# Kernel tuning notes

Hardware: AMD Instinct MI355X
Metric: run time of the kernel (lower is better)

The kernel has to match this reference:

```python
import jax, jax.numpy as jnp
import numpy as np

PC_LO = jnp.array([-50.0, -50.0, -5.0], jnp.float32)
PC_HI = jnp.array([50.0, 50.0, 3.0], jnp.float32)
IMG_H, IMG_W = 256, 704
G, P, L = 1, 8, 4
C_FEAT = 132  # 128 feat + 3 pos_3d + 1 uncertainty
ALPHA, EPS = 0.1, 1e-6


def conv2d(x, w, b, pad):
    y = jax.lax.conv_general_dilated(x, w, (1, 1), [(pad, pad), (pad, pad)],
                                     dimension_numbers=('NCHW', 'OIHW', 'NCHW'))
    return y + b[None, :, None, None]


def inorm(x, eps=1e-5):
    m = x.mean(axis=(2, 3), keepdims=True)
    v = ((x - m) ** 2).mean(axis=(2, 3), keepdims=True)
    return (x - m) * jax.lax.rsqrt(v + eps)


def bilinear_sample(feat, gx, gy):
    # feat [C,H,W]; gx,gy [Q] in [-1,1]; align_corners=False, zero padding
    C, H, W = feat.shape
    x = (gx + 1.0) * 0.5 * W - 0.5
    y = (gy + 1.0) * 0.5 * H - 0.5
    x0 = jnp.floor(x)
    y0 = jnp.floor(y)
    wx1 = x - x0
    wy1 = y - y0

    def tap(xi, yi, wgt):
        ok = (xi >= 0) & (xi < W) & (yi >= 0) & (yi < H)
        xi_c = jnp.clip(xi, 0, W - 1).astype(jnp.int32)
        yi_c = jnp.clip(yi, 0, H - 1).astype(jnp.int32)
        return feat[:, yi_c, xi_c] * (wgt * ok)[None, :]

    return (tap(x0, y0, (1 - wx1) * (1 - wy1)) + tap(x0 + 1, y0, wx1 * (1 - wy1))
            + tap(x0, y0 + 1, (1 - wx1) * wy1) + tap(x0 + 1, y0 + 1, wx1 * wy1))


def reference(bev_query, bev_pos, lidar2img, feat0, feat1, feat2, feat3,
              in_w, in_b, off_w, off_b, sw_w, sw_b,
              mid_w1, mid_b1, mid_w2, mid_b2, mid_w3, mid_b3, out_w, out_b):
    b, _, h, w = bev_query.shape
    hw = h * w
    scale = 1.0
    # in_conv + InstanceNorm
    q = bev_query + conv2d(bev_query, in_w, in_b, 2)
    q = inorm(q)
    # sampling offsets: b (g p 3) h w -> b (h w) g p 3
    off = jax.nn.sigmoid(conv2d(q, off_w, off_b, 0))
    off = off.reshape(b, G, P, 3, h, w).transpose(0, 4, 5, 1, 2, 3).reshape(b, hw, G, P, 3)
    rng = 0.25 * scale + EPS
    off = jnp.concatenate([off[..., :2] * rng * 2 - rng,
                           off[..., 2:3] * (4.0 + EPS) * 2 - (4.0 + EPS)], axis=-1)
    # reference points: normalized bev_pos -> metric + offsets
    ref = bev_pos.reshape(b, hw, 1, 1, 3) * (PC_HI - PC_LO) + PC_LO
    ref = ref + off  # [b, hw, g, p, 3]
    # scale weights: b (g p l) h w -> b (h w) g 1 p l, softmax over l
    sw = conv2d(q, sw_w, sw_b, 0).reshape(b, G, P, L, h, w)
    sw = sw.transpose(0, 4, 5, 1, 2, 3).reshape(b, hw, G, P, L)[:, :, :, None]
    sw = jax.nn.softmax(sw, axis=-1)
    # sampling_4d: project 3D points to each camera
    pts = jnp.concatenate([ref, jnp.ones(ref.shape[:-1] + (1,), ref.dtype)], axis=-1)
    cam = jnp.einsum('bnij,bqgpj->bnqgpi', lidar2img, pts)  # [b,n,hw,g,p,4]
    z = cam[..., 2]
    valid = z > 1e-5
    xy = cam[..., :2] / jnp.maximum(z, 1e-5)[..., None]
    gx = jnp.where(valid, xy[..., 0] / IMG_W * 2 - 1, -2.0)
    gy = jnp.where(valid, xy[..., 1] / IMG_H * 2 - 1, -2.0)
    n = lidar2img.shape[1]
    Q = hw * G * P
    gxf = gx.reshape(b * n, Q)
    gyf = gy.reshape(b * n, Q)
    sampled = jnp.zeros((b, n, hw, G, P, C_FEAT), ref.dtype)
    for l, feat in enumerate((feat0, feat1, feat2, feat3)):
        ff = feat.reshape(b * n, C_FEAT, feat.shape[3], feat.shape[4])
        s = jax.vmap(bilinear_sample)(ff, gxf, gyf)  # [bn, C, Q]
        s = s.reshape(b, n, C_FEAT, hw, G, P).transpose(0, 1, 3, 4, 5, 2)
        wl = sw[:, :, :, 0, :, l]  # [b, hw, g, p]
        sampled = sampled + s * wl[:, None, :, :, :, None]
    sampled = sampled.sum(axis=1)  # sum over cameras -> [b, hw, g, p, C_FEAT]
    # split: 128 features, 3 pos_3d, 1 uncertainty
    feats128 = sampled[..., :128]
    pos3d = sampled[..., 128:131]
    dist = jnp.linalg.norm(ref - pos3d, axis=-1)
    wgt = jnp.exp(-ALPHA * dist ** 2)[..., None]
    weighted = feats128 * wgt

    def fold(x):  # b (h w) g p c -> b p (g c) h w -> sum over p
        return x.reshape(b, h, w, G * P, 128).sum(axis=3).transpose(0, 3, 1, 2)

    sf = jnp.concatenate([fold(feats128), fold(weighted)], axis=1)  # [b,256,h,w]
    m = jax.nn.gelu(conv2d(sf, mid_w1, mid_b1, 1), approximate=False)
    m = jax.nn.gelu(conv2d(m, mid_w2, mid_b2, 0), approximate=False)
    q = q + conv2d(m, mid_w3, mid_b3, 1)
    q = inorm(q)
    q = q + conv2d(q, out_w, out_b, 2)
    q = inorm(q)
    return q


def setup_inputs():
    key = jax.random.key(0)
    ks = jax.random.split(key, 32)
    f32 = jnp.float32
    d = {}
    d['bev_query'] = jax.random.normal(ks[0], (1, 128, 100, 100), f32)
    d['bev_pos'] = jax.random.uniform(ks[1], (1, 100, 100, 3), f32)
    d['lidar2img'] = jax.random.normal(ks[2], (1, 6, 4, 4), f32)
    lvl_shapes = [(32, 88), (16, 44), (8, 22), (4, 11)]
    for i, (hh, ww) in enumerate(lvl_shapes):
        d['feat%d' % i] = jax.random.normal(ks[3 + i], (1, 6, C_FEAT, hh, ww), f32)

    def W(k, shape):
        return jax.random.normal(k, shape, f32) * 0.05

    d['in_w'] = W(ks[10], (128, 128, 5, 5)); d['in_b'] = W(ks[11], (128,))
    d['off_w'] = W(ks[12], (G * P * 3, 128, 1, 1))
    d['off_b'] = jax.random.uniform(ks[13], (G * P * 3,), f32, -2.0, 2.0)
    d['sw_w'] = W(ks[14], (G * P * L, 128, 1, 1)); d['sw_b'] = W(ks[15], (G * P * L,))
    d['mid_w1'] = W(ks[16], (512, 256, 3, 3)); d['mid_b1'] = W(ks[17], (512,))
    d['mid_w2'] = W(ks[18], (512, 512, 1, 1)); d['mid_b2'] = W(ks[19], (512,))
    d['mid_w3'] = W(ks[20], (128, 512, 3, 3)); d['mid_b3'] = W(ks[21], (128,))
    d['out_w'] = W(ks[22], (128, 128, 5, 5)); d['out_b'] = W(ks[23], (128,))
    return d
```

## Files before the change

kernel.cpp:

```cpp
#include <hip/hip_runtime.h>
#include <cstddef>


#define HW   10000
#define WID  100

typedef __attribute__((ext_vector_type(8))) __bf16 bf16x8;
typedef __attribute__((ext_vector_type(4))) float f32x4;
typedef __attribute__((ext_vector_type(4))) unsigned int uint4v;

#define AS1 __attribute__((address_space(1)))
#define AS3 __attribute__((address_space(3)))

__device__ __forceinline__ float gelu_exact(float x) {
    return 0.5f * x * (1.0f + erff(x * 0.7071067811865475f));
}
__device__ __forceinline__ unsigned short f2bf(float v) {
    unsigned int b = __float_as_uint(v);
    return (unsigned short)((b + 0x7FFFu + ((b >> 16) & 1u)) >> 16);
}
__device__ __forceinline__ float bf2f(short s) {
    return __uint_as_float(((unsigned int)(unsigned short)s) << 16);
}
__device__ __forceinline__ bf16x8 load_frag(const short* p) {
    return __builtin_bit_cast(bf16x8, *(const uint4v*)p);
}

template<int CIN, int KS, int COUT, int EPI, bool ACT, int OPAD, int OPW, int KSPLIT>
__global__ __launch_bounds__(256)
void mfma_conv(const short* __restrict__ wpk, const short* __restrict__ xcl,
               const float* __restrict__ bias,
               float* __restrict__ outcm, short* __restrict__ outcl)
{
    constexpr int PW = 100 + 2 * (KS / 2);
    constexpr int CHUNK = (KS + KSPLIT - 1) / KSPLIT;
    constexpr int CINB = CIN / 32;
    __shared__ short As[8192];
    __shared__ short Bs[8192];

    const int t    = threadIdx.x;
    const int lane = t & 63;
    const int wv   = t >> 6;
    const int wr = wv >> 1;
    const int wc = wv & 1;
    const int lq = lane >> 4;
    const int ln = lane & 15;

    const int oc0 = blockIdx.x * 128;
    const int y0  = blockIdx.y * 4;
    const int zb  = blockIdx.z;
    const int bx  = (KSPLIT > 1) ? (zb & 3) : zb;
    const int ks  = (KSPLIT > 1) ? (zb >> 2) : 0;
    const int x0  = bx * 32;
    const int ky_lo = ks * CHUNK;
    const int ky_hi = (ky_lo + CHUNK < KS) ? ky_lo + CHUNK : KS;

    const int srow  = t >> 2;
    const int sslot = (t & 3) * 8;

    const int nsteps = (ky_hi - ky_lo) * KS * CINB;

    f32x4 acc[4][4];
#pragma unroll
    for (int mt = 0; mt < 4; ++mt)
#pragma unroll
        for (int nt = 0; nt < 4; ++nt)
#pragma unroll
            for (int r = 0; r < 4; ++r) acc[mt][nt][r] = 0.f;

    auto stage = [&](int b, int s) {
        const int ky  = ky_lo + s / (KS * CINB);
        const int rem = s % (KS * CINB);
        const int kx  = rem / CINB;
        const int ic0 = (rem % CINB) * 32;
        const short* wsl = wpk + (size_t)((ky * KS + kx) * COUT + oc0) * CIN + ic0 + sslot;
        const short* xsl = xcl + (size_t)(ky * PW + kx) * CIN + ic0 + sslot;
#pragma unroll
        for (int i = 0; i < 2; ++i) {
            const int row = i * 64 + srow;
            const short* ga = wsl + (size_t)row * CIN;
            __builtin_amdgcn_global_load_lds(
                (const AS1 unsigned int*)ga,
                (AS3 unsigned int*)((AS3 char*)As + b * 8192 + i * 4096 + wv * 1024),
                16, 0, 0);
        }
#pragma unroll
        for (int i = 0; i < 2; ++i) {
            const int np = i * 64 + srow;
            const short* gb = xsl + (size_t)((y0 + (np >> 5)) * PW + x0 + (np & 31)) * CIN;
            __builtin_amdgcn_global_load_lds(
                (const AS1 unsigned int*)gb,
                (AS3 unsigned int*)((AS3 char*)Bs + b * 8192 + i * 4096 + wv * 1024),
                16, 0, 0);
        }
    };

    stage(0, 0);
    __syncthreads();

    int cur = 0;
    for (int s = 0; s < nsteps; ++s) {
        if (s + 1 < nsteps) stage(cur ^ 1, s + 1);

        const short* ab = As + cur * 4096;
        const short* bb = Bs + cur * 4096;
        bf16x8 a[4], b[4];
#pragma unroll
        for (int mt = 0; mt < 4; ++mt)
            a[mt] = load_frag(ab + (wr * 64 + mt * 16 + ln) * 32 + lq * 8);
#pragma unroll
        for (int nt = 0; nt < 4; ++nt)
            b[nt] = load_frag(bb + (wc * 64 + nt * 16 + ln) * 32 + lq * 8);
#pragma unroll
        for (int mt = 0; mt < 4; ++mt)
#pragma unroll
            for (int nt = 0; nt < 4; ++nt)
                acc[mt][nt] = __builtin_amdgcn_mfma_f32_16x16x32_bf16(
                    a[mt], b[nt], acc[mt][nt], 0, 0, 0);

        __syncthreads();
        cur ^= 1;
    }

#pragma unroll
    for (int mt = 0; mt < 4; ++mt) {
        const int ocr = oc0 + wr * 64 + mt * 16 + lq * 4;
        float bb[4];
        if (EPI == 1) {
            const float4 bv = *(const float4*)(bias + ocr);
            bb[0] = bv.x; bb[1] = bv.y; bb[2] = bv.z; bb[3] = bv.w;
        }
#pragma unroll
        for (int nt = 0; nt < 4; ++nt) {
            const int nl = wc * 64 + nt * 16 + ln;
            const int x = x0 + (nl & 31);
            const int y = y0 + (nl >> 5);
            if (x >= 100) continue;
            if (EPI == 1) {
                float v[4];
#pragma unroll
                for (int r = 0; r < 4; ++r) {
                    float tv = acc[mt][nt][r] + bb[r];
                    if (ACT) tv = gelu_exact(tv);
                    v[r] = tv;
                }
                ushort4 pk;
                pk.x = f2bf(v[0]); pk.y = f2bf(v[1]); pk.z = f2bf(v[2]); pk.w = f2bf(v[3]);
                *(ushort4*)(outcl + ((size_t)(y + OPAD) * OPW + (x + OPAD)) * COUT + ocr) = pk;
            } else {
                const int pix = y * WID + x;
#pragma unroll
                for (int r = 0; r < 4; ++r)
                    outcm[((size_t)ks * COUT + ocr + r) * HW + pix] = acc[mt][nt][r];
            }
        }
    }
}

template<int NS>
__global__ __launch_bounds__(256)
void red_norm_k(const float* __restrict__ bias, const float* __restrict__ res,
                const float* __restrict__ slab, float* __restrict__ outp)
{
    const int c = blockIdx.x, tid = threadIdx.x;
    const size_t base = (size_t)c * HW;
    const float bc = bias[c];
    float v[40];
    float s1 = 0.f, s2 = 0.f;
#pragma unroll
    for (int k = 0; k < 40; ++k) {
        const int i = tid + k * 256;
        float x = 0.f;
        if (i < HW) {
            x = bc + res[base + i];
#pragma unroll
            for (int z = 0; z < NS; ++z) x += slab[(size_t)z * 1280000 + base + i];
            s1 += x; s2 += x * x;
        }
        v[k] = x;
    }
    __shared__ float r1[256], r2[256];
    r1[tid] = s1; r2[tid] = s2; __syncthreads();
    for (int o = 128; o > 0; o >>= 1) {
        if (tid < o) { r1[tid] += r1[tid + o]; r2[tid] += r2[tid + o]; }
        __syncthreads();
    }
    const float mean = r1[0] * 1e-4f;
    const float var  = fmaxf(r2[0] * 1e-4f - mean * mean, 0.f);
    const float rstd = rsqrtf(var + 1e-5f);
#pragma unroll
    for (int k = 0; k < 40; ++k) {
        const int i = tid + k * 256;
        if (i < HW) outp[base + i] = (v[k] - mean) * rstd;
    }
}

__global__ void pad_cat_x(const float* __restrict__ in, short* __restrict__ out)
{
    const int total = 10816 * 384;
    for (int i = blockIdx.x * blockDim.x + threadIdx.x; i < total; i += gridDim.x * blockDim.x) {
        const int c = i % 384;
        const int p = i / 384;
        const int x = p % 104 - 2;
        const int y = p / 104 - 2;
        const int sc = c & 127;
        float v = 0.f;
        if (x >= 0 && x < 100 && y >= 0 && y < 100) v = in[(size_t)sc * HW + y * WID + x];
        const unsigned short hi = f2bf(v);
        short o;
        if (c >= 128 && c < 256) o = (short)f2bf(v - bf2f((short)hi));
        else                     o = (short)hi;
        out[i] = o;
    }
}

__global__ void pack_w1_cat(const float* __restrict__ w, short* __restrict__ out)
{
    const int total = 25 * 128 * 384;
    for (int i = blockIdx.x * blockDim.x + threadIdx.x; i < total; i += gridDim.x * blockDim.x) {
        const int c = i % 384;
        int t = i / 384;
        const int oc = t % 128;
        const int s = t / 128;
        const int ky = s / 5, kx = s % 5;
        const int sc = c & 127;
        const float v = w[(((size_t)oc * 128 + sc) * 5 + ky) * 5 + kx];
        const unsigned short hi = f2bf(v);
        out[i] = (c < 256) ? (short)hi : (short)f2bf(v - bf2f((short)hi));
    }
}

template<int C, int PAD>
__global__ void pad_cl_cast(const float* __restrict__ in, short* __restrict__ out)
{
    constexpr int PW = 100 + 2 * PAD;
    const int total = PW * PW * C;
    for (int i = blockIdx.x * blockDim.x + threadIdx.x; i < total; i += gridDim.x * blockDim.x) {
        const int c = i % C;
        const int p = i / C;
        const int x = p % PW - PAD;
        const int y = p / PW - PAD;
        float v = 0.f;
        if (x >= 0 && x < 100 && y >= 0 && y < 100) v = in[(size_t)c * HW + y * WID + x];
        out[i] = (short)f2bf(v);
    }
}

__global__ void pack_all_bf16(const float* __restrict__ w1, const float* __restrict__ w2,
                              const float* __restrict__ w3, const float* __restrict__ w4,
                              short* __restrict__ out)
{
    const int E0 = 1179648, E1 = E0 + 262144, E2 = E1 + 589824, E3 = E2 + 409600;
    for (int i = blockIdx.x * blockDim.x + threadIdx.x; i < E3; i += gridDim.x * blockDim.x) {
        const float* w; int OC, CI, KS, j;
        if (i < E0)      { w = w1; OC = 512; CI = 256; KS = 3; j = i; }
        else if (i < E1) { w = w2; OC = 512; CI = 512; KS = 1; j = i - E0; }
        else if (i < E2) { w = w3; OC = 128; CI = 512; KS = 3; j = i - E1; }
        else             { w = w4; OC = 128; CI = 128; KS = 5; j = i - E2; }
        const int ic = j % CI;
        int t = j / CI;
        const int oc = t % OC;
        const int s = t / OC;
        const int ky = s / KS, kx = s % KS;
        out[i] = (short)f2bf(w[(((size_t)oc * CI + ic) * KS + ky) * KS + kx]);
    }
}

__global__ void transpose_all(const float* __restrict__ f0, const float* __restrict__ f1,
                              const float* __restrict__ f2, const float* __restrict__ f3,
                              short* __restrict__ out)
{
    const int O1 = 2230272, O2 = O1 + 557568, O3 = O2 + 139392, O4 = O3 + 34848;
    for (int i = blockIdx.x * blockDim.x + threadIdx.x; i < O4; i += gridDim.x * blockDim.x) {
        const float* f; int Hl, Wl, j;
        if (i < O1)      { f = f0; Hl = 32; Wl = 88; j = i; }
        else if (i < O2) { f = f1; Hl = 16; Wl = 44; j = i - O1; }
        else if (i < O3) { f = f2; Hl = 8;  Wl = 22; j = i - O2; }
        else             { f = f3; Hl = 4;  Wl = 11; j = i - O3; }
        const int c = j % 132;
        int t = j / 132;
        const int x = t % Wl; t /= Wl;
        const int y = t % Hl; t /= Hl;
        const int n = t;
        out[i] = (short)f2bf(f[(((size_t)n * 132 + c) * Hl + y) * Wl + x]);
    }
}

__global__ __launch_bounds__(64)
void offsw_proj(const float* __restrict__ qn, const float* __restrict__ bev_pos,
                const float* __restrict__ off_w, const float* __restrict__ off_b,
                const float* __restrict__ sw_w, const float* __restrict__ sw_b,
                const float* __restrict__ l2i,
                float* __restrict__ refp, float* __restrict__ swts,
                float2* __restrict__ recs, int* __restrict__ recn, int* __restrict__ cnts)
{
    const int pix = blockIdx.x;
    const int tid = threadIdx.x;
    __shared__ float qv[128];
    __shared__ float swraw[32];
    __shared__ float rp[24];
    qv[tid]      = qn[(size_t)tid * HW + pix];
    qv[tid + 64] = qn[(size_t)(tid + 64) * HW + pix];
    __syncthreads();

    if (tid < 24) {
        float acc = off_b[tid];
        for (int c = 0; c < 128; ++c) acc = fmaf(qv[c], off_w[tid * 128 + c], acc);
        const float s = 1.0f / (1.0f + expf(-acc));
        const int coord = tid % 3;
        const float rng = (coord < 2) ? 0.250001f : 4.000001f;
        const float v = s * rng * 2.0f - rng;
        const float lo[3]   = {-50.f, -50.f, -5.f};
        const float span[3] = {100.f, 100.f, 8.f};
        const float rv = bev_pos[pix * 3 + coord] * span[coord] + lo[coord] + v;
        refp[pix * 24 + tid] = rv;
        rp[tid] = rv;
    } else if (tid >= 32) {
        const int j = tid - 32;
        float acc = sw_b[j];
        for (int c = 0; c < 128; ++c) acc = fmaf(qv[c], sw_w[j * 128 + c], acc);
        swraw[j] = acc;
    }
    __syncthreads();
    if (tid < 8) {
        float m = -1e30f;
#pragma unroll
        for (int l = 0; l < 4; ++l) m = fmaxf(m, swraw[tid * 4 + l]);
        float e[4], sum = 0.f;
#pragma unroll
        for (int l = 0; l < 4; ++l) { e[l] = expf(swraw[tid * 4 + l] - m); sum += e[l]; }
        const float inv = 1.0f / sum;
#pragma unroll
        for (int l = 0; l < 4; ++l) swts[pix * 32 + tid * 4 + l] = e[l] * inv;
    }

    bool keep = false;
    float gx = -2.f, gy = -2.f;
    int p = 0, n = 0;
    if (tid < 48) {
        p = tid / 6;
        n = tid - p * 6;
        const float X = rp[p * 3 + 0], Y = rp[p * 3 + 1], Z = rp[p * 3 + 2];
        const float* m = l2i + n * 16;
        const float cx = m[0] * X + m[1] * Y + m[2]  * Z + m[3];
        const float cy = m[4] * X + m[5] * Y + m[6]  * Z + m[7];
        const float cz = m[8] * X + m[9] * Y + m[10] * Z + m[11];
        const bool valid = cz > 1e-5f;
        const float zz = fmaxf(cz, 1e-5f);
        gx = valid ? (cx / zz) * (2.0f / 704.0f) - 1.0f : -2.0f;
        gy = valid ? (cy / zz) * (2.0f / 256.0f) - 1.0f : -2.0f;
        keep = (gx > -1.092f) && (gx < 1.092f) && (gy > -1.26f) && (gy < 1.26f);
    }
    const unsigned long long bm = __ballot(keep);
    if (keep) {
        const unsigned long long gmask = 0x3Full << (p * 6);
        const int slot = __popcll(bm & ((1ull << tid) - 1ull) & gmask);
        recs[(size_t)pix * 48 + p * 6 + slot] = make_float2(gx, gy);
        recn[(size_t)pix * 48 + p * 6 + slot] = n;
    }
    if (tid < 48 && (tid % 6) == 0) {
        const unsigned long long gmask = 0x3Full << (p * 6);
        cnts[pix * 8 + p] = __popcll(bm & gmask);
    }
}

__global__ __launch_bounds__(64)
void sample_k4(const float* __restrict__ refp, const float* __restrict__ swts,
               const float2* __restrict__ recs, const int* __restrict__ recn,
               const int* __restrict__ cnts,
               const short* __restrict__ fb0,
               short* __restrict__ sfo)
{
    const int pix = blockIdx.x;
    const int tid = threadIdx.x;
    const int c0  = tid * 2;
    __shared__ float rp[24], sw[32], tail[32];
    __shared__ float2 rec[48];
    __shared__ int rn[48];
    __shared__ int cnt[8];
    __shared__ int4   toff[192];
    __shared__ float4 twt[192];
    if (tid < 24) rp[tid] = refp[pix * 24 + tid];
    if (tid < 32) sw[tid] = swts[pix * 32 + tid];
    if (tid < 48) { rec[tid] = recs[(size_t)pix * 48 + tid]; rn[tid] = recn[(size_t)pix * 48 + tid]; }
    if (tid < 8)  cnt[tid] = cnts[pix * 8 + tid];
    __syncthreads();

    const int HL[4] = {32, 16, 8, 4};
    const int WL[4] = {88, 44, 22, 11};
    const int LB[4] = {0, 2230272, 2787840, 2927232};

    for (int e = tid; e < 192; e += 64) {
        const int p  = e / 24;
        const int rl = e - p * 24;
        const int r  = rl >> 2;
        const int l  = rl & 3;
        int4 off = make_int4(0, 0, 0, 0);
        float4 wt = make_float4(0.f, 0.f, 0.f, 0.f);
        if (r < cnt[p]) {
            const float gx = rec[p * 6 + r].x;
            const float gy = rec[p * 6 + r].y;
            const int   n  = rn[p * 6 + r];
            const float wl = sw[p * 4 + l];
            const int Hl = HL[l], Wl = WL[l];
            const float fx = (gx + 1.0f) * 0.5f * (float)Wl - 0.5f;
            const float fy = (gy + 1.0f) * 0.5f * (float)Hl - 0.5f;
            if (fx >= -1.0f && fx < (float)Wl && fy >= -1.0f && fy < (float)Hl) {
                const float x0f = floorf(fx), y0f = floorf(fy);
                const int x0 = (int)x0f, y0 = (int)y0f;
                const int x1 = x0 + 1, y1 = y0 + 1;
                const float wx1 = fx - x0f, wy1 = fy - y0f;
                const float wx0 = 1.0f - wx1, wy0 = 1.0f - wy1;
                const bool okx0 = (x0 >= 0), okx1 = (x1 < Wl);
                const bool oky0 = (y0 >= 0), oky1 = (y1 < Hl);
                const int xc0 = okx0 ? x0 : 0, xc1 = okx1 ? x1 : Wl - 1;
                const int yc0 = oky0 ? y0 : 0, yc1 = oky1 ? y1 : Hl - 1;
                const int base = LB[l] + n * Hl * Wl * 132;
                off.x = base + (yc0 * Wl + xc0) * 132;
                off.y = base + (yc0 * Wl + xc1) * 132;
                off.z = base + (yc1 * Wl + xc0) * 132;
                off.w = base + (yc1 * Wl + xc1) * 132;
                wt.x = (okx0 && oky0) ? wx0 * wy0 * wl : 0.f;
                wt.y = (okx1 && oky0) ? wx1 * wy0 * wl : 0.f;
                wt.z = (okx0 && oky1) ? wx0 * wy1 * wl : 0.f;
                wt.w = (okx1 && oky1) ? wx1 * wy1 * wl : 0.f;
            }
        }
        toff[e] = off;
        twt[e]  = wt;
    }
    __syncthreads();

#define LOADB(L, W, P, R)                                                        \
    do {                                                                         \
        const int eb_ = (P) * 24 + (R) * 4;                                      \
        _Pragma("unroll")                                                        \
        for (int l = 0; l < 4; ++l) {                                            \
            const int4 offv_ = toff[eb_ + l];                                    \
            W[l] = twt[eb_ + l];                                                 \
            const int ox_ = __builtin_amdgcn_readfirstlane(offv_.x);             \
            const int oy_ = __builtin_amdgcn_readfirstlane(offv_.y);             \
            const int oz_ = __builtin_amdgcn_readfirstlane(offv_.z);             \
            const int ow_ = __builtin_amdgcn_readfirstlane(offv_.w);             \
            L[l * 4 + 0] = *(const unsigned int*)(fb0 + ox_ + c0);               \
            L[l * 4 + 1] = *(const unsigned int*)(fb0 + oy_ + c0);               \
            L[l * 4 + 2] = *(const unsigned int*)(fb0 + oz_ + c0);               \
            L[l * 4 + 3] = *(const unsigned int*)(fb0 + ow_ + c0);               \
        }                                                                        \
    } while (0)

#define FMAB(L, W)                                                               \
    do {                                                                         \
        _Pragma("unroll")                                                        \
        for (int l = 0; l < 4; ++l) {                                            \
            a0.x = fmaf(__uint_as_float(L[l * 4 + 0] << 16),          W[l].x, a0.x); \
            a0.y = fmaf(__uint_as_float(L[l * 4 + 0] & 0xFFFF0000u),  W[l].x, a0.y); \
            a1.x = fmaf(__uint_as_float(L[l * 4 + 1] << 16),          W[l].y, a1.x); \
            a1.y = fmaf(__uint_as_float(L[l * 4 + 1] & 0xFFFF0000u),  W[l].y, a1.y); \
            a2.x = fmaf(__uint_as_float(L[l * 4 + 2] << 16),          W[l].z, a2.x); \
            a2.y = fmaf(__uint_as_float(L[l * 4 + 2] & 0xFFFF0000u),  W[l].z, a2.y); \
            a3.x = fmaf(__uint_as_float(L[l * 4 + 3] << 16),          W[l].w, a3.x); \
            a3.y = fmaf(__uint_as_float(L[l * 4 + 3] & 0xFFFF0000u),  W[l].w, a3.y); \
        }                                                                        \
    } while (0)

    float2 acc[8];
#pragma unroll
    for (int p = 0; p < 8; ++p) {
        float2 a0 = {0.f, 0.f}, a1 = {0.f, 0.f}, a2 = {0.f, 0.f}, a3 = {0.f, 0.f};
        const int c = cnt[p];
        unsigned int LA[16]; float4 WA[4];
        if (c > 0) LOADB(LA, WA, p, 0);
        int r = 0;
        while (r < c) {
            unsigned int LB2[16]; float4 WB[4];
            if (r + 1 < c) LOADB(LB2, WB, p, r + 1);
            FMAB(LA, WA);
            ++r;
            if (r >= c) break;
            if (r + 1 < c) LOADB(LA, WA, p, r + 1);
            FMAB(LB2, WB);
            ++r;
        }
        acc[p].x = (a0.x + a1.x) + (a2.x + a3.x);
        acc[p].y = (a0.y + a1.y) + (a2.y + a3.y);
    }
#undef LOADB
#undef FMAB

    {
        const int p   = tid >> 3;
        const int sub = tid & 7;
        const int c   = cnt[p];
        const int nslots = c * 16;
        float t0 = 0.f, t1 = 0.f, t2 = 0.f;
        for (int s = sub; s < nslots; s += 8) {
            const int e  = p * 24 + (s >> 2);
            const int tp = s & 3;
            const int4   offv = toff[e];
            const float4 wtv  = twt[e];
            const int   off = (tp == 0) ? offv.x : (tp == 1) ? offv.y : (tp == 2) ? offv.z : offv.w;
            const float w   = (tp == 0) ? wtv.x  : (tp == 1) ? wtv.y  : (tp == 2) ? wtv.z  : wtv.w;
            const uint2 u = *(const uint2*)(fb0 + off + 128);
            t0 = fmaf(__uint_as_float(u.x << 16),         w, t0);
            t1 = fmaf(__uint_as_float(u.x & 0xFFFF0000u), w, t1);
            t2 = fmaf(__uint_as_float(u.y << 16),         w, t2);
        }
#pragma unroll
        for (int o = 4; o > 0; o >>= 1) {
            t0 += __shfl_down(t0, o, 8);
            t1 += __shfl_down(t1, o, 8);
            t2 += __shfl_down(t2, o, 8);
        }
        if (sub == 0) {
            tail[p * 4 + 0] = t0;
            tail[p * 4 + 1] = t1;
            tail[p * 4 + 2] = t2;
        }
    }
    __syncthreads();

    float2 sf1 = {0.f, 0.f}, sf2 = {0.f, 0.f};
#pragma unroll
    for (int p = 0; p < 8; ++p) {
        const float dx = rp[p * 3]     - tail[p * 4 + 0];
        const float dy = rp[p * 3 + 1] - tail[p * 4 + 1];
        const float dz = rp[p * 3 + 2] - tail[p * 4 + 2];
        const float wgt = expf(-0.1f * (dx * dx + dy * dy + dz * dz));
        sf1.x += acc[p].x;  sf1.y += acc[p].y;
        sf2.x += acc[p].x * wgt;  sf2.y += acc[p].y * wgt;
    }
    const int y = pix / WID, x = pix % WID;
    const size_t po = ((size_t)(y + 1) * 102 + (x + 1)) * 256;
    ushort2 p1; p1.x = f2bf(sf1.x); p1.y = f2bf(sf1.y);
    ushort2 p2; p2.x = f2bf(sf2.x); p2.y = f2bf(sf2.y);
    *(ushort2*)(sfo + po + c0)       = p1;
    *(ushort2*)(sfo + po + 128 + c0) = p2;
}


extern "C" void kernel_launch(void* const* d_in, const int* in_sizes, int n_in,
                              void* d_out, int out_size, void* d_ws, size_t ws_size,
                              hipStream_t stream)
{
    const float* bev_query = (const float*)d_in[0];
    const float* bev_pos   = (const float*)d_in[1];
    const float* l2i       = (const float*)d_in[2];
    const float* feat0     = (const float*)d_in[3];
    const float* feat1     = (const float*)d_in[4];
    const float* feat2     = (const float*)d_in[5];
    const float* feat3     = (const float*)d_in[6];
    const float* in_w      = (const float*)d_in[7];
    const float* in_b      = (const float*)d_in[8];
    const float* off_w     = (const float*)d_in[9];
    const float* off_b     = (const float*)d_in[10];
    const float* sw_w      = (const float*)d_in[11];
    const float* sw_b      = (const float*)d_in[12];
    const float* mid_w1    = (const float*)d_in[13];
    const float* mid_b1    = (const float*)d_in[14];
    const float* mid_w2    = (const float*)d_in[15];
    const float* mid_b2    = (const float*)d_in[16];
    const float* mid_w3    = (const float*)d_in[17];
    const float* mid_b3    = (const float*)d_in[18];
    const float* out_w     = (const float*)d_in[19];
    const float* out_b     = (const float*)d_in[20];
    float* out = (float*)d_out;

    float* ws    = (float*)d_ws;
    float* qn    = ws;
    float* refp  = qn + 1280000;
    float* swts  = refp + 240000;
    float* E     = swts + 320000;
    float* F     = E + 6400000;
    float* H     = F + 1800000;
    short* wp_all= (short*)(H + 2700000);

    float*  slab  = E;
    short*  fT0   = (short*)E;
    float2* recs  = (float2*)(E + 1600000);
    int*    recn  = (int*)(E + 2560000);
    int*    cnts  = (int*)(E + 3040000);
    short*  m1_cl = (short*)E;
    short*  xcat  = (short*)F;
    short*  wcat  = (short*)(F + 2100000);
    short*  sf_cl = (short*)F;
    short*  q2pad = (short*)F;
    short*  m2_cl = (short*)H;
    short*  wp_m1 = wp_all;
    short*  wp_m2 = wp_m1 + 1179648;
    short*  wp_m3 = wp_m2 + 262144;
    short*  wp_out= wp_m3 + 589824;

    const dim3 blk(256);

    hipLaunchKernelGGL(pack_w1_cat, dim3(1200), blk, 0, stream, in_w, wcat);
    hipLaunchKernelGGL(pack_all_bf16, dim3(9536), blk, 0, stream,
                       mid_w1, mid_w2, mid_w3, out_w, wp_all);

    hipLaunchKernelGGL(pad_cat_x, dim3(4056), blk, 0, stream, bev_query, xcat);
    hipLaunchKernelGGL((mfma_conv<384, 5, 128, 2, false, 0, 0, 5>), dim3(1, 25, 20), blk, 0, stream,
                       wcat, xcat, in_b, slab, nullptr);
    hipLaunchKernelGGL(red_norm_k<5>, dim3(128), blk, 0, stream, in_b, bev_query, slab, qn);

    hipLaunchKernelGGL(offsw_proj, dim3(HW), dim3(64), 0, stream,
                       qn, bev_pos, off_w, off_b, sw_w, sw_b, l2i,
                       refp, swts, recs, recn, cnts);

    hipLaunchKernelGGL(transpose_all, dim3(11571), blk, 0, stream,
                       feat0, feat1, feat2, feat3, fT0);

    hipMemsetAsync(sf_cl, 0, (size_t)2663424 * 2, stream);
    hipLaunchKernelGGL(sample_k4, dim3(HW), dim3(64), 0, stream,
                       refp, swts, recs, recn, cnts, fT0, sf_cl);

    hipLaunchKernelGGL((mfma_conv<256, 3, 512, 1, true, 0, 100, 1>), dim3(4, 25, 4), blk, 0, stream,
                       wp_m1, sf_cl, mid_b1, nullptr, m1_cl);
    hipMemsetAsync(m2_cl, 0, (size_t)5326848 * 2, stream);
    hipLaunchKernelGGL((mfma_conv<512, 1, 512, 1, true, 1, 102, 1>), dim3(4, 25, 4), blk, 0, stream,
                       wp_m2, m1_cl, mid_b2, nullptr, m2_cl);
    hipLaunchKernelGGL((mfma_conv<512, 3, 128, 2, false, 0, 0, 3>), dim3(1, 25, 12), blk, 0, stream,
                       wp_m3, m2_cl, mid_b3, slab, nullptr);
    hipLaunchKernelGGL(red_norm_k<3>, dim3(128), blk, 0, stream, mid_b3, qn, slab, qn);
    hipLaunchKernelGGL((pad_cl_cast<128, 2>), dim3(5411), blk, 0, stream, qn, q2pad);
    hipLaunchKernelGGL((mfma_conv<128, 5, 128, 2, false, 0, 0, 5>), dim3(1, 25, 20), blk, 0, stream,
                       wp_out, q2pad, out_b, slab, nullptr);
    hipLaunchKernelGGL(red_norm_k<5>, dim3(128), blk, 0, stream, out_b, qn, slab, out);
}
```

Before: 528.0 us.

## Halve conv pixel tile to two rows and interleave sampling of two points

The MFMA conv template gains an NT parameter. All five conv launches now use a 2-row pixel tile (64 pixels) instead of 4 rows, which doubles the grid, halves accumulator registers and B-tile LDS, and should raise occupancy on a 256-CU part. In exchange, weight tiles are reloaded twice as often per output. Separately, the sampling kernel processes two sampling points per loop iteration with interleaved loads and FMAs for more memory-level parallelism. It also reads weights from LDS at FMA time instead of holding them in registers.

```diff
diff --git a/kernel.cpp b/kernel.cpp
--- a/kernel.cpp
+++ b/kernel.cpp
@@ -26,7 +26,7 @@
     return __builtin_bit_cast(bf16x8, *(const uint4v*)p);
 }
 
-template<int CIN, int KS, int COUT, int EPI, bool ACT, int OPAD, int OPW, int KSPLIT>
+template<int CIN, int KS, int COUT, int EPI, bool ACT, int OPAD, int OPW, int KSPLIT, int NT>
 __global__ __launch_bounds__(256)
 void mfma_conv(const short* __restrict__ wpk, const short* __restrict__ xcl,
                const float* __restrict__ bias,
@@ -35,8 +35,9 @@
     constexpr int PW = 100 + 2 * (KS / 2);
     constexpr int CHUNK = (KS + KSPLIT - 1) / KSPLIT;
     constexpr int CINB = CIN / 32;
+    constexpr int BBUF = NT * 2048;
     __shared__ short As[8192];
-    __shared__ short Bs[8192];
+    __shared__ short Bs[NT * 2048];
 
     const int t    = threadIdx.x;
     const int lane = t & 63;
@@ -47,7 +48,7 @@
     const int ln = lane & 15;
 
     const int oc0 = blockIdx.x * 128;
-    const int y0  = blockIdx.y * 4;
+    const int y0  = blockIdx.y * NT;
     const int zb  = blockIdx.z;
     const int bx  = (KSPLIT > 1) ? (zb & 3) : zb;
     const int ks  = (KSPLIT > 1) ? (zb >> 2) : 0;
@@ -60,11 +61,11 @@
 
     const int nsteps = (ky_hi - ky_lo) * KS * CINB;
 
-    f32x4 acc[4][4];
+    f32x4 acc[4][NT];
 #pragma unroll
     for (int mt = 0; mt < 4; ++mt)
 #pragma unroll
-        for (int nt = 0; nt < 4; ++nt)
+        for (int nt = 0; nt < NT; ++nt)
 #pragma unroll
             for (int r = 0; r < 4; ++r) acc[mt][nt][r] = 0.f;
 
@@ -85,12 +86,12 @@
                 16, 0, 0);
         }
 #pragma unroll
-        for (int i = 0; i < 2; ++i) {
+        for (int i = 0; i < NT / 2; ++i) {
             const int np = i * 64 + srow;
             const short* gb = xsl + (size_t)((y0 + (np >> 5)) * PW + x0 + (np & 31)) * CIN;
             __builtin_amdgcn_global_load_lds(
                 (const AS1 unsigned int*)gb,
-                (AS3 unsigned int*)((AS3 char*)Bs + b * 8192 + i * 4096 + wv * 1024),
+                (AS3 unsigned int*)((AS3 char*)Bs + b * BBUF + i * 4096 + wv * 1024),
                 16, 0, 0);
         }
     };
@@ -103,18 +104,18 @@
         if (s + 1 < nsteps) stage(cur ^ 1, s + 1);
 
         const short* ab = As + cur * 4096;
-        const short* bb = Bs + cur * 4096;
-        bf16x8 a[4], b[4];
+        const short* bb = Bs + cur * (NT * 1024);
+        bf16x8 a[4], b[NT];
 #pragma unroll
         for (int mt = 0; mt < 4; ++mt)
             a[mt] = load_frag(ab + (wr * 64 + mt * 16 + ln) * 32 + lq * 8);
 #pragma unroll
-        for (int nt = 0; nt < 4; ++nt)
-            b[nt] = load_frag(bb + (wc * 64 + nt * 16 + ln) * 32 + lq * 8);
+        for (int nt = 0; nt < NT; ++nt)
+            b[nt] = load_frag(bb + (wc * (NT * 16) + nt * 16 + ln) * 32 + lq * 8);
 #pragma unroll
         for (int mt = 0; mt < 4; ++mt)
 #pragma unroll
-            for (int nt = 0; nt < 4; ++nt)
+            for (int nt = 0; nt < NT; ++nt)
                 acc[mt][nt] = __builtin_amdgcn_mfma_f32_16x16x32_bf16(
                     a[mt], b[nt], acc[mt][nt], 0, 0, 0);
 
@@ -131,8 +132,8 @@
             bb[0] = bv.x; bb[1] = bv.y; bb[2] = bv.z; bb[3] = bv.w;
         }
 #pragma unroll
-        for (int nt = 0; nt < 4; ++nt) {
-            const int nl = wc * 64 + nt * 16 + ln;
+        for (int nt = 0; nt < NT; ++nt) {
+            const int nl = wc * (NT * 16) + nt * 16 + ln;
             const int x = x0 + (nl & 31);
             const int y = y0 + (nl >> 5);
             if (x >= 100) continue;
@@ -431,13 +432,12 @@
     }
     __syncthreads();
 
-#define LOADB(L, W, P, R)                                                        \
+#define LOADD(L, P, R)                                                           \
     do {                                                                         \
         const int eb_ = (P) * 24 + (R) * 4;                                      \
         _Pragma("unroll")                                                        \
         for (int l = 0; l < 4; ++l) {                                            \
             const int4 offv_ = toff[eb_ + l];                                    \
-            W[l] = twt[eb_ + l];                                                 \
             const int ox_ = __builtin_amdgcn_readfirstlane(offv_.x);             \
             const int oy_ = __builtin_amdgcn_readfirstlane(offv_.y);             \
             const int oz_ = __builtin_amdgcn_readfirstlane(offv_.z);             \
@@ -449,44 +449,51 @@
         }                                                                        \
     } while (0)
 
-#define FMAB(L, W)                                                               \
+#define FMAW(A0, A1, A2, A3, L, P, R)                                            \
     do {                                                                         \
+        const int eb_ = (P) * 24 + (R) * 4;                                      \
         _Pragma("unroll")                                                        \
         for (int l = 0; l < 4; ++l) {                                            \
-            a0.x = fmaf(__uint_as_float(L[l * 4 + 0] << 16),          W[l].x, a0.x); \
-            a0.y = fmaf(__uint_as_float(L[l * 4 + 0] & 0xFFFF0000u),  W[l].x, a0.y); \
-            a1.x = fmaf(__uint_as_float(L[l * 4 + 1] << 16),          W[l].y, a1.x); \
-            a1.y = fmaf(__uint_as_float(L[l * 4 + 1] & 0xFFFF0000u),  W[l].y, a1.y); \
-            a2.x = fmaf(__uint_as_float(L[l * 4 + 2] << 16),          W[l].z, a2.x); \
-            a2.y = fmaf(__uint_as_float(L[l * 4 + 2] & 0xFFFF0000u),  W[l].z, a2.y); \
-            a3.x = fmaf(__uint_as_float(L[l * 4 + 3] << 16),          W[l].w, a3.x); \
-            a3.y = fmaf(__uint_as_float(L[l * 4 + 3] & 0xFFFF0000u),  W[l].w, a3.y); \
+            const float4 w_ = twt[eb_ + l];                                      \
+            A0.x = fmaf(__uint_as_float(L[l * 4 + 0] << 16),          w_.x, A0.x); \
+            A0.y = fmaf(__uint_as_float(L[l * 4 + 0] & 0xFFFF0000u),  w_.x, A0.y); \
+            A1.x = fmaf(__uint_as_float(L[l * 4 + 1] << 16),          w_.y, A1.x); \
+            A1.y = fmaf(__uint_as_float(L[l * 4 + 1] & 0xFFFF0000u),  w_.y, A1.y); \
+            A2.x = fmaf(__uint_as_float(L[l * 4 + 2] << 16),          w_.z, A2.x); \
+            A2.y = fmaf(__uint_as_float(L[l * 4 + 2] & 0xFFFF0000u),  w_.z, A2.y); \
+            A3.x = fmaf(__uint_as_float(L[l * 4 + 3] << 16),          w_.w, A3.x); \
+            A3.y = fmaf(__uint_as_float(L[l * 4 + 3] & 0xFFFF0000u),  w_.w, A3.y); \
         }                                                                        \
     } while (0)
 
     float2 acc[8];
 #pragma unroll
-    for (int p = 0; p < 8; ++p) {
-        float2 a0 = {0.f, 0.f}, a1 = {0.f, 0.f}, a2 = {0.f, 0.f}, a3 = {0.f, 0.f};
-        const int c = cnt[p];
-        unsigned int LA[16]; float4 WA[4];
-        if (c > 0) LOADB(LA, WA, p, 0);
-        int r = 0;
-        while (r < c) {
-            unsigned int LB2[16]; float4 WB[4];
-            if (r + 1 < c) LOADB(LB2, WB, p, r + 1);
-            FMAB(LA, WA);
-            ++r;
-            if (r >= c) break;
-            if (r + 1 < c) LOADB(LA, WA, p, r + 1);
-            FMAB(LB2, WB);
-            ++r;
-        }
-        acc[p].x = (a0.x + a1.x) + (a2.x + a3.x);
-        acc[p].y = (a0.y + a1.y) + (a2.y + a3.y);
-    }
-#undef LOADB
-#undef FMAB
+    for (int q = 0; q < 4; ++q) {
+        const int pA = q * 2, pB = q * 2 + 1;
+        const int cA = cnt[pA], cB = cnt[pB];
+        const int cM = (cA > cB) ? cA : cB;
+        float2 xA0 = {0.f, 0.f}, xA1 = {0.f, 0.f}, xA2 = {0.f, 0.f}, xA3 = {0.f, 0.f};
+        float2 xB0 = {0.f, 0.f}, xB1 = {0.f, 0.f}, xB2 = {0.f, 0.f}, xB3 = {0.f, 0.f};
+        unsigned int LA0[16], LB0[16], LA1[16], LB1[16];
+        if (cA > 0) LOADD(LA0, pA, 0);
+        if (cB > 0) LOADD(LB0, pB, 0);
+        for (int r = 0; r < cM; r += 2) {
+            if (r + 1 < cA) LOADD(LA1, pA, r + 1);
+            if (r + 1 < cB) LOADD(LB1, pB, r + 1);
+            if (r < cA) FMAW(xA0, xA1, xA2, xA3, LA0, pA, r);
+            if (r < cB) FMAW(xB0, xB1, xB2, xB3, LB0, pB, r);
+            if (r + 2 < cA) LOADD(LA0, pA, r + 2);
+            if (r + 2 < cB) LOADD(LB0, pB, r + 2);
+            if (r + 1 < cA) FMAW(xA0, xA1, xA2, xA3, LA1, pA, r + 1);
+            if (r + 1 < cB) FMAW(xB0, xB1, xB2, xB3, LB1, pB, r + 1);
+        }
+        acc[pA].x = (xA0.x + xA1.x) + (xA2.x + xA3.x);
+        acc[pA].y = (xA0.y + xA1.y) + (xA2.y + xA3.y);
+        acc[pB].x = (xB0.x + xB1.x) + (xB2.x + xB3.x);
+        acc[pB].y = (xB0.y + xB1.y) + (xB2.y + xB3.y);
+    }
+#undef LOADD
+#undef FMAW
 
     {
         const int p   = tid >> 3;
@@ -598,7 +605,7 @@
                        mid_w1, mid_w2, mid_w3, out_w, wp_all);
 
     hipLaunchKernelGGL(pad_cat_x, dim3(4056), blk, 0, stream, bev_query, xcat);
-    hipLaunchKernelGGL((mfma_conv<384, 5, 128, 2, false, 0, 0, 5>), dim3(1, 25, 20), blk, 0, stream,
+    hipLaunchKernelGGL((mfma_conv<384, 5, 128, 2, false, 0, 0, 5, 2>), dim3(1, 50, 20), blk, 0, stream,
                        wcat, xcat, in_b, slab, nullptr);
     hipLaunchKernelGGL(red_norm_k<5>, dim3(128), blk, 0, stream, in_b, bev_query, slab, qn);
 
@@ -613,16 +620,16 @@
     hipLaunchKernelGGL(sample_k4, dim3(HW), dim3(64), 0, stream,
                        refp, swts, recs, recn, cnts, fT0, sf_cl);
 
-    hipLaunchKernelGGL((mfma_conv<256, 3, 512, 1, true, 0, 100, 1>), dim3(4, 25, 4), blk, 0, stream,
+    hipLaunchKernelGGL((mfma_conv<256, 3, 512, 1, true, 0, 100, 1, 2>), dim3(4, 50, 4), blk, 0, stream,
                        wp_m1, sf_cl, mid_b1, nullptr, m1_cl);
     hipMemsetAsync(m2_cl, 0, (size_t)5326848 * 2, stream);
-    hipLaunchKernelGGL((mfma_conv<512, 1, 512, 1, true, 1, 102, 1>), dim3(4, 25, 4), blk, 0, stream,
+    hipLaunchKernelGGL((mfma_conv<512, 1, 512, 1, true, 1, 102, 1, 2>), dim3(4, 50, 4), blk, 0, stream,
                        wp_m2, m1_cl, mid_b2, nullptr, m2_cl);
-    hipLaunchKernelGGL((mfma_conv<512, 3, 128, 2, false, 0, 0, 3>), dim3(1, 25, 12), blk, 0, stream,
+    hipLaunchKernelGGL((mfma_conv<512, 3, 128, 2, false, 0, 0, 3, 2>), dim3(1, 50, 12), blk, 0, stream,
                        wp_m3, m2_cl, mid_b3, slab, nullptr);
     hipLaunchKernelGGL(red_norm_k<3>, dim3(128), blk, 0, stream, mid_b3, qn, slab, qn);
     hipLaunchKernelGGL((pad_cl_cast<128, 2>), dim3(5411), blk, 0, stream, qn, q2pad);
-    hipLaunchKernelGGL((mfma_conv<128, 5, 128, 2, false, 0, 0, 5>), dim3(1, 25, 20), blk, 0, stream,
+    hipLaunchKernelGGL((mfma_conv<128, 5, 128, 2, false, 0, 0, 5, 2>), dim3(1, 50, 20), blk, 0, stream,
                        wp_out, q2pad, out_b, slab, nullptr);
     hipLaunchKernelGGL(red_norm_k<5>, dim3(128), blk, 0, stream, out_b, qn, slab, out);
 }
```

After: 523.9 us. No clear change (-0.8%).

## Halve conv pixel tile and double K-step depth per barrier in MFMA conv

Applied to the files above, without the earlier changes.

The MFMA conv kernel gains an NT template parameter that sets the pixel tile height. All launches use NT=2, which halves the N tile from 128 to 64 pixels and doubles the grid along y. Each pipeline stage now loads two 32-channel slices (64 input channels) before a barrier, so there are half as many syncthreads per unit of K work. The aim is more blocks for occupancy and fewer barriers. The cost is less weight reuse per block, because A is reloaded for half as many pixels, plus more LDS for A.

```diff
diff --git a/kernel.cpp b/kernel.cpp
--- a/kernel.cpp
+++ b/kernel.cpp
@@ -26,7 +26,7 @@
     return __builtin_bit_cast(bf16x8, *(const uint4v*)p);
 }
 
-template<int CIN, int KS, int COUT, int EPI, bool ACT, int OPAD, int OPW, int KSPLIT>
+template<int CIN, int KS, int COUT, int EPI, bool ACT, int OPAD, int OPW, int KSPLIT, int NT>
 __global__ __launch_bounds__(256)
 void mfma_conv(const short* __restrict__ wpk, const short* __restrict__ xcl,
                const float* __restrict__ bias,
@@ -34,9 +34,9 @@
 {
     constexpr int PW = 100 + 2 * (KS / 2);
     constexpr int CHUNK = (KS + KSPLIT - 1) / KSPLIT;
-    constexpr int CINB = CIN / 32;
-    __shared__ short As[8192];
-    __shared__ short Bs[8192];
+    constexpr int CINB2 = CIN / 64;
+    __shared__ short As[16384];
+    __shared__ short Bs[NT * 4096];
 
     const int t    = threadIdx.x;
     const int lane = t & 63;
@@ -47,7 +47,7 @@
     const int ln = lane & 15;
 
     const int oc0 = blockIdx.x * 128;
-    const int y0  = blockIdx.y * 4;
+    const int y0  = blockIdx.y * NT;
     const int zb  = blockIdx.z;
     const int bx  = (KSPLIT > 1) ? (zb & 3) : zb;
     const int ks  = (KSPLIT > 1) ? (zb >> 2) : 0;
@@ -58,40 +58,44 @@
     const int srow  = t >> 2;
     const int sslot = (t & 3) * 8;
 
-    const int nsteps = (ky_hi - ky_lo) * KS * CINB;
-
-    f32x4 acc[4][4];
+    const int nsteps = (ky_hi - ky_lo) * KS * CINB2;
+
+    f32x4 acc[4][NT];
 #pragma unroll
     for (int mt = 0; mt < 4; ++mt)
 #pragma unroll
-        for (int nt = 0; nt < 4; ++nt)
+        for (int nt = 0; nt < NT; ++nt)
 #pragma unroll
             for (int r = 0; r < 4; ++r) acc[mt][nt][r] = 0.f;
 
     auto stage = [&](int b, int s) {
-        const int ky  = ky_lo + s / (KS * CINB);
-        const int rem = s % (KS * CINB);
-        const int kx  = rem / CINB;
-        const int ic0 = (rem % CINB) * 32;
-        const short* wsl = wpk + (size_t)((ky * KS + kx) * COUT + oc0) * CIN + ic0 + sslot;
-        const short* xsl = xcl + (size_t)(ky * PW + kx) * CIN + ic0 + sslot;
-#pragma unroll
-        for (int i = 0; i < 2; ++i) {
-            const int row = i * 64 + srow;
-            const short* ga = wsl + (size_t)row * CIN;
-            __builtin_amdgcn_global_load_lds(
-                (const AS1 unsigned int*)ga,
-                (AS3 unsigned int*)((AS3 char*)As + b * 8192 + i * 4096 + wv * 1024),
-                16, 0, 0);
-        }
-#pragma unroll
-        for (int i = 0; i < 2; ++i) {
-            const int np = i * 64 + srow;
-            const short* gb = xsl + (size_t)((y0 + (np >> 5)) * PW + x0 + (np & 31)) * CIN;
-            __builtin_amdgcn_global_load_lds(
-                (const AS1 unsigned int*)gb,
-                (AS3 unsigned int*)((AS3 char*)Bs + b * 8192 + i * 4096 + wv * 1024),
-                16, 0, 0);
+        const int ky  = ky_lo + s / (KS * CINB2);
+        const int rem = s % (KS * CINB2);
+        const int kx  = rem / CINB2;
+        const int ic0 = (rem % CINB2) * 64;
+#pragma unroll
+        for (int u = 0; u < 2; ++u) {
+            const short* wsl = wpk + (size_t)((ky * KS + kx) * COUT + oc0) * CIN
+                               + ic0 + u * 32 + sslot;
+            const short* xsl = xcl + (size_t)(ky * PW + kx) * CIN + ic0 + u * 32 + sslot;
+#pragma unroll
+            for (int i = 0; i < 2; ++i) {
+                const int row = i * 64 + srow;
+                const short* ga = wsl + (size_t)row * CIN;
+                __builtin_amdgcn_global_load_lds(
+                    (const AS1 unsigned int*)ga,
+                    (AS3 unsigned int*)((AS3 char*)As + (b * 2 + u) * 8192 + i * 4096 + wv * 1024),
+                    16, 0, 0);
+            }
+#pragma unroll
+            for (int i = 0; i < NT / 2; ++i) {
+                const int np = i * 64 + srow;
+                const short* gb = xsl + (size_t)((y0 + (np >> 5)) * PW + x0 + (np & 31)) * CIN;
+                __builtin_amdgcn_global_load_lds(
+                    (const AS1 unsigned int*)gb,
+                    (AS3 unsigned int*)((AS3 char*)Bs + (b * 2 + u) * (NT * 2048) + i * 4096 + wv * 1024),
+                    16, 0, 0);
+            }
         }
     };
 
@@ -102,21 +106,24 @@
     for (int s = 0; s < nsteps; ++s) {
         if (s + 1 < nsteps) stage(cur ^ 1, s + 1);
 
-        const short* ab = As + cur * 4096;
-        const short* bb = Bs + cur * 4096;
-        bf16x8 a[4], b[4];
-#pragma unroll
-        for (int mt = 0; mt < 4; ++mt)
-            a[mt] = load_frag(ab + (wr * 64 + mt * 16 + ln) * 32 + lq * 8);
-#pragma unroll
-        for (int nt = 0; nt < 4; ++nt)
-            b[nt] = load_frag(bb + (wc * 64 + nt * 16 + ln) * 32 + lq * 8);
-#pragma unroll
-        for (int mt = 0; mt < 4; ++mt)
-#pragma unroll
-            for (int nt = 0; nt < 4; ++nt)
-                acc[mt][nt] = __builtin_amdgcn_mfma_f32_16x16x32_bf16(
-                    a[mt], b[nt], acc[mt][nt], 0, 0, 0);
+#pragma unroll
+        for (int u = 0; u < 2; ++u) {
+            const short* ab = As + (cur * 2 + u) * 4096;
+            const short* bb = Bs + (cur * 2 + u) * (NT * 1024);
+            bf16x8 a[4], b[NT];
+#pragma unroll
+            for (int mt = 0; mt < 4; ++mt)
+                a[mt] = load_frag(ab + (wr * 64 + mt * 16 + ln) * 32 + lq * 8);
+#pragma unroll
+            for (int nt = 0; nt < NT; ++nt)
+                b[nt] = load_frag(bb + (wc * (NT * 16) + nt * 16 + ln) * 32 + lq * 8);
+#pragma unroll
+            for (int mt = 0; mt < 4; ++mt)
+#pragma unroll
+                for (int nt = 0; nt < NT; ++nt)
+                    acc[mt][nt] = __builtin_amdgcn_mfma_f32_16x16x32_bf16(
+                        a[mt], b[nt], acc[mt][nt], 0, 0, 0);
+        }
 
         __syncthreads();
         cur ^= 1;
@@ -131,8 +138,8 @@
             bb[0] = bv.x; bb[1] = bv.y; bb[2] = bv.z; bb[3] = bv.w;
         }
 #pragma unroll
-        for (int nt = 0; nt < 4; ++nt) {
-            const int nl = wc * 64 + nt * 16 + ln;
+        for (int nt = 0; nt < NT; ++nt) {
+            const int nl = wc * (NT * 16) + nt * 16 + ln;
             const int x = x0 + (nl & 31);
             const int y = y0 + (nl >> 5);
             if (x >= 100) continue;
@@ -598,7 +605,7 @@
                        mid_w1, mid_w2, mid_w3, out_w, wp_all);
 
     hipLaunchKernelGGL(pad_cat_x, dim3(4056), blk, 0, stream, bev_query, xcat);
-    hipLaunchKernelGGL((mfma_conv<384, 5, 128, 2, false, 0, 0, 5>), dim3(1, 25, 20), blk, 0, stream,
+    hipLaunchKernelGGL((mfma_conv<384, 5, 128, 2, false, 0, 0, 5, 2>), dim3(1, 50, 20), blk, 0, stream,
                        wcat, xcat, in_b, slab, nullptr);
     hipLaunchKernelGGL(red_norm_k<5>, dim3(128), blk, 0, stream, in_b, bev_query, slab, qn);
 
@@ -613,16 +620,16 @@
     hipLaunchKernelGGL(sample_k4, dim3(HW), dim3(64), 0, stream,
                        refp, swts, recs, recn, cnts, fT0, sf_cl);
 
-    hipLaunchKernelGGL((mfma_conv<256, 3, 512, 1, true, 0, 100, 1>), dim3(4, 25, 4), blk, 0, stream,
+    hipLaunchKernelGGL((mfma_conv<256, 3, 512, 1, true, 0, 100, 1, 2>), dim3(4, 50, 4), blk, 0, stream,
                        wp_m1, sf_cl, mid_b1, nullptr, m1_cl);
     hipMemsetAsync(m2_cl, 0, (size_t)5326848 * 2, stream);
-    hipLaunchKernelGGL((mfma_conv<512, 1, 512, 1, true, 1, 102, 1>), dim3(4, 25, 4), blk, 0, stream,
+    hipLaunchKernelGGL((mfma_conv<512, 1, 512, 1, true, 1, 102, 1, 2>), dim3(4, 50, 4), blk, 0, stream,
                        wp_m2, m1_cl, mid_b2, nullptr, m2_cl);
-    hipLaunchKernelGGL((mfma_conv<512, 3, 128, 2, false, 0, 0, 3>), dim3(1, 25, 12), blk, 0, stream,
+    hipLaunchKernelGGL((mfma_conv<512, 3, 128, 2, false, 0, 0, 3, 2>), dim3(1, 50, 12), blk, 0, stream,
                        wp_m3, m2_cl, mid_b3, slab, nullptr);
     hipLaunchKernelGGL(red_norm_k<3>, dim3(128), blk, 0, stream, mid_b3, qn, slab, qn);
     hipLaunchKernelGGL((pad_cl_cast<128, 2>), dim3(5411), blk, 0, stream, qn, q2pad);
-    hipLaunchKernelGGL((mfma_conv<128, 5, 128, 2, false, 0, 0, 5>), dim3(1, 25, 20), blk, 0, stream,
+    hipLaunchKernelGGL((mfma_conv<128, 5, 128, 2, false, 0, 0, 5, 2>), dim3(1, 50, 20), blk, 0, stream,
                        wp_out, q2pad, out_b, slab, nullptr);
     hipLaunchKernelGGL(red_norm_k<5>, dim3(128), blk, 0, stream, out_b, qn, slab, out);
 }
```

Result: slower. 548.1 us (+3.8%).
